# Kernel tuning notes

Measured on AMD Instinct MI355X. Metric: run time of the kernel, lower is better.

## Reference

```python
import jax, jax.numpy as jnp
import numpy as np
import math

NHEADS = 8


def pos_encoding_2d(d_model, H, W):
    dm = d_model // 2
    div = jnp.exp(jnp.arange(0, dm, 2, dtype=jnp.float32) * (-math.log(10000.0) / dm))  # [dm//2]
    pw = jnp.arange(W, dtype=jnp.float32)[:, None] * div  # [W, dm//2]
    ph = jnp.arange(H, dtype=jnp.float32)[:, None] * div  # [H, dm//2]
    pe = jnp.zeros((d_model, H, W), jnp.float32)
    pe = pe.at[0:dm:2].set(jnp.broadcast_to(jnp.sin(pw).T[:, None, :], (dm // 2, H, W)))
    pe = pe.at[1:dm:2].set(jnp.broadcast_to(jnp.cos(pw).T[:, None, :], (dm // 2, H, W)))
    pe = pe.at[dm::2].set(jnp.broadcast_to(jnp.sin(ph).T[:, :, None], (dm // 2, H, W)))
    pe = pe.at[dm + 1::2].set(jnp.broadcast_to(jnp.cos(ph).T[:, :, None], (dm // 2, H, W)))
    return pe


def conv_same(x, w, b):
    y = jax.lax.conv_general_dilated(x, w, (1, 1), 'SAME',
                                     dimension_numbers=('NCHW', 'OIHW', 'NCHW'))
    return y + b[None, :, None, None]


def layernorm(x, g, b, eps=1e-5):
    mu = x.mean(-1, keepdims=True)
    var = ((x - mu) ** 2).mean(-1, keepdims=True)
    return (x - mu) / jnp.sqrt(var + eps) * g + b


def setup_inputs() -> dict:
    key = jax.random.key(0)
    B, C, H, W = 8, 256, 32, 32
    KQV, NH, K = 64, NHEADS, 3
    ks = jax.random.split(key, 16)
    s_conv = 1.0 / math.sqrt(C * K * K)
    s_lin = 1.0 / math.sqrt(NH * KQV)
    s_ff = 1.0 / math.sqrt(C)
    return {
        'x': jax.random.normal(ks[0], (B, C, H, W), jnp.float32),
        'Wk': jax.random.normal(ks[1], (NH * KQV, C, K, K), jnp.float32) * s_conv,
        'bk': jax.random.normal(ks[2], (NH * KQV,), jnp.float32) * s_conv,
        'Wq': jax.random.normal(ks[3], (NH * KQV, C, K, K), jnp.float32) * s_conv,
        'bq': jax.random.normal(ks[4], (NH * KQV,), jnp.float32) * s_conv,
        'Wv': jax.random.normal(ks[5], (NH * KQV, C, K, K), jnp.float32) * s_conv,
        'bv': jax.random.normal(ks[6], (NH * KQV,), jnp.float32) * s_conv,
        'Wproj': jax.random.normal(ks[7], (C, NH * KQV), jnp.float32) * s_lin,
        'bproj': jax.random.normal(ks[8], (C,), jnp.float32) * s_lin,
        'ln_g': jnp.ones((C,), jnp.float32),
        'ln_b': jnp.zeros((C,), jnp.float32),
        'W1': jax.random.normal(ks[9], (C, C), jnp.float32) * s_ff,
        'b1': jax.random.normal(ks[10], (C,), jnp.float32) * s_ff,
        'W2': jax.random.normal(ks[11], (C, C), jnp.float32) * s_ff,
        'b2': jax.random.normal(ks[12], (C,), jnp.float32) * s_ff,
    }


def reference(x, Wk, bk, Wq, bq, Wv, bv, Wproj, bproj, ln_g, ln_b, W1, b1, W2, b2):
    B, C, H, W = x.shape
    N = H * W
    pe = pos_encoding_2d(C, H, W)
    xp = x + pe[None]                                   # [B,C,H,W]
    xflat = xp.reshape(B, C, N).transpose(0, 2, 1)      # [B,N,C]

    def heads(w, b):
        return conv_same(xp, w, b).reshape(B, NHEADS, -1, N)  # [B,h,c,N]

    k = heads(Wk, bk)
    q = heads(Wq, bq)
    v = heads(Wv, bv)
    scores = jnp.einsum('bhcn,bhcm->bhnm', k, q) / N    # K^T Q / N, [B,h,N,N]
    sm = jax.nn.softmax(scores, axis=1)                 # Softmax2d -> over HEAD dim (faithful)
    att = jnp.einsum('bhnm,bhcm->bhnc', sm, v)          # [B,h,N,c]
    att = att.transpose(0, 2, 3, 1).reshape(B, N, -1)   # [B,N,c*h] (channel-major, head-minor)
    attproj = att @ Wproj.T + bproj                     # [B,N,C]
    addnormed = layernorm(xflat + attproj, ln_g, ln_b)
    h1 = addnormed @ W1.T + b1
    h1 = jnp.where(h1 > 0, h1, 0.1 * h1)                # LeakyReLU(0.1)
    h2 = h1 @ W2.T + b2
    out = layernorm(h2 + addnormed, ln_g, ln_b)         # same LN params reused (faithful)
    return out.transpose(0, 2, 1).reshape(B, C, H, W)
```

## Files before the change

### kernel.cpp

```cpp
#include <hip/hip_runtime.h>
#include <stdint.h>

typedef __attribute__((ext_vector_type(8))) short short8;
typedef __attribute__((ext_vector_type(4))) short s16x4;
typedef __attribute__((ext_vector_type(4))) float f32x4;

#define DEVI __device__ __forceinline__

#if __has_builtin(__builtin_amdgcn_mfma_f32_16x16x16_bf16)
#define MFMA16(a, b, c) __builtin_amdgcn_mfma_f32_16x16x16_bf16(a, b, c, 0, 0, 0)
#else
#define MFMA16(a, b, c) __builtin_amdgcn_mfma_f32_16x16x16bf16_1k(a, b, c, 0, 0, 0)
#endif

DEVI unsigned short f2bf(float f) {
  union { float f; uint32_t u; } v; v.f = f;
  return (unsigned short)((v.u + 0x7fffu + ((v.u >> 16) & 1u)) >> 16);
}

DEVI float bf2f(uint32_t hi16) {
  union { uint32_t u; float f; } v; v.u = hi16;
  return v.f;
}

DEVI uint32_t pkbf(float a, float b) {
  union { float f; uint32_t u; } x, y; x.f = a; y.f = b;
  return ((x.u + 0x8000u) >> 16) | (((y.u + 0x8000u) >> 16) << 16);
}

DEVI void gload_lds16(const void* g, void* l) {
  __builtin_amdgcn_global_load_lds(
      (const __attribute__((address_space(1))) uint32_t*)g,
      (__attribute__((address_space(3))) uint32_t*)l, 16, 0, 0);
}

__global__ void k_petab(float* __restrict__ T, float* __restrict__ zp) {
  int c = threadIdx.x;
  zp[c] = 0.0f;
  int idx = ((c >= 128) ? c - 128 : c) >> 1;
  float freq = expf(-(float)idx * (logf(10000.0f) / 64.0f));
  for (int p = 0; p < 32; ++p) {
    float ang = (float)p * freq;
    T[c * 32 + p] = (c & 1) ? cosf(ang) : sinf(ang);
  }
}

__global__ __launch_bounds__(256) void k_xpt(const float* __restrict__ x,
                                             const float* __restrict__ T,
                                             unsigned short* __restrict__ xpt_bf,
                                             float* __restrict__ xpt_f) {
  __shared__ __align__(16) float tile[32][36];
  const int b = blockIdx.z, c0 = blockIdx.x * 32, n0 = blockIdx.y * 32;
  const int t = threadIdx.x;
  {
    const int cl = t >> 3, ng = (t & 7) * 4;
    const int c = c0 + cl;
    float4 v = *(const float4*)(x + ((size_t)b * 256 + c) * 1024 + n0 + ng);
    float p0, p1, p2, p3;
    if (c < 128) {
      p0 = T[c * 32 + ng + 0]; p1 = T[c * 32 + ng + 1];
      p2 = T[c * 32 + ng + 2]; p3 = T[c * 32 + ng + 3];
    } else {
      p0 = p1 = p2 = p3 = T[c * 32 + (n0 >> 5)];
    }
    tile[ng + 0][cl] = v.x + p0;
    tile[ng + 1][cl] = v.y + p1;
    tile[ng + 2][cl] = v.z + p2;
    tile[ng + 3][cl] = v.w + p3;
  }
  __syncthreads();
  {
    const int nl = t >> 3, cg = (t & 7) * 4;
    float o0 = tile[nl][cg + 0], o1 = tile[nl][cg + 1];
    float o2 = tile[nl][cg + 2], o3 = tile[nl][cg + 3];
    size_t row = (size_t)b * 1024 + n0 + nl;
    *(float4*)(xpt_f + row * 256 + c0 + cg) = make_float4(o0, o1, o2, o3);
    uint32_t lo = (uint32_t)f2bf(o0) | ((uint32_t)f2bf(o1) << 16);
    uint32_t hi = (uint32_t)f2bf(o2) | ((uint32_t)f2bf(o3) << 16);
    *(uint2*)(xpt_bf + row * 256 + c0 + cg) = make_uint2(lo, hi);
  }
}

__global__ void k_packw(const float* __restrict__ Wk, const float* __restrict__ Wq,
                        const float* __restrict__ Wv, unsigned short* __restrict__ Wpack) {
  int i = blockIdx.x * 256 + threadIdx.x;
  if (i >= 1536 * 2304) return;
  int o = i / 2304, kn = i % 2304;
  int ci = kn & 255, khw = kn >> 8;
  const float* src = (o < 512) ? Wk : ((o < 1024) ? Wq : Wv);
  int oo = o & 511;
  Wpack[i] = f2bf(src[((size_t)oo * 256 + ci) * 9 + khw]);
}

__global__ void k_packmisc(const float* __restrict__ bk, const float* __restrict__ bq,
                           const float* __restrict__ bv, const float* __restrict__ Wproj,
                           const float* __restrict__ W1, const float* __restrict__ W2,
                           float* __restrict__ bias_kqv, unsigned short* __restrict__ WprojP,
                           unsigned short* __restrict__ W1b, unsigned short* __restrict__ W2b) {
  int i = blockIdx.x * 256 + threadIdx.x;
  if (i < 1536)
    bias_kqv[i] = (i < 512) ? bk[i] : ((i < 1024) ? bq[i - 512] : bv[i - 1024]);
  if (i < 131072) {
    int j = i >> 9, f = i & 511;
    int h = f >> 6, c = f & 63;
    WprojP[i] = f2bf(Wproj[(size_t)j * 512 + c * 8 + h]);
  }
  if (i < 65536) {
    W1b[i] = f2bf(W1[i]);
    W2b[i] = f2bf(W2[i]);
  }
}

__global__ __launch_bounds__(256, 2) void k_gemm_conv(const unsigned short* __restrict__ xpt,
                                                      const unsigned short* __restrict__ Wp,
                                                      unsigned short* __restrict__ kqv,
                                                      const float* __restrict__ bias,
                                                      const char* __restrict__ zp) {
  __shared__ __align__(16) unsigned short As[2][128 * 64];
  __shared__ __align__(16) unsigned short Bs[2][128 * 64];
  const int tid = threadIdx.x, l = tid & 63, w = tid >> 6;
  const int wm = w >> 1, wn = w & 1, g = l >> 4, ln = l & 15;
  const int m0 = blockIdx.x * 128, n0 = blockIdx.y * 128;
  const int swz = (l & 7) ^ (l >> 3);

  int rA[4];
  const char* pAbase[4];
  const char* pA[4];
#pragma unroll
  for (int j = 0; j < 4; ++j) {
    int r = m0 + (w * 4 + j) * 8 + (l >> 3);
    rA[j] = r;
    pAbase[j] = (const char*)xpt + ((size_t)r * 256 + swz * 8) * 2;
  }
  const char* pB[4];
#pragma unroll
  for (int j = 0; j < 4; ++j) {
    int r = n0 + (w * 4 + j) * 8 + (l >> 3);
    pB[j] = (const char*)Wp + ((size_t)r * 2304 + swz * 8) * 2;
  }

  f32x4 acc[4][4] = {};

  auto setA = [&](int khw) {
    int d3 = (khw * 11) >> 5;
    int dy = d3 - 1, dx = khw - d3 * 3 - 1;
    int off = (dy * 32 + dx) * 512;
#pragma unroll
    for (int j = 0; j < 4; ++j) {
      int y = ((rA[j] >> 5) & 31) + dy;
      int x = (rA[j] & 31) + dx;
      pA[j] = (((unsigned)y < 32u) && ((unsigned)x < 32u)) ? (pAbase[j] + off) : zp;
    }
  };
  auto STAGE = [&](int buf) {
#pragma unroll
    for (int j = 0; j < 4; ++j) {
      gload_lds16(pA[j], (char*)As + buf * 16384 + (w * 4 + j) * 1024);
      pA[j] += 128;
    }
#pragma unroll
    for (int j = 0; j < 4; ++j) {
      gload_lds16(pB[j], (char*)Bs + buf * 16384 + (w * 4 + j) * 1024);
      pB[j] += 128;
    }
  };
  auto COMPUTE = [&](int buf) {
    const char* Ab2 = (const char*)As + buf * 16384;
    const char* Bb2 = (const char*)Bs + buf * 16384;
#pragma unroll
    for (int kk = 0; kk < 2; ++kk) {
      short8 af[4], bfr[4];
#pragma unroll
      for (int fm = 0; fm < 4; ++fm)
        af[fm] = *(const short8*)(Ab2 + (wm * 64 + fm * 16 + ln) * 128 +
                                  (((kk * 4 + g) ^ (ln & 7)) * 16));
#pragma unroll
      for (int fn = 0; fn < 4; ++fn)
        bfr[fn] = *(const short8*)(Bb2 + (wn * 64 + fn * 16 + ln) * 128 +
                                   (((kk * 4 + g) ^ (ln & 7)) * 16));
#pragma unroll
      for (int fm = 0; fm < 4; ++fm)
#pragma unroll
        for (int fn = 0; fn < 4; ++fn)
          acc[fm][fn] = __builtin_amdgcn_mfma_f32_16x16x32_bf16(af[fm], bfr[fn], acc[fm][fn], 0, 0, 0);
    }
  };

  setA(0);
  STAGE(0);
#pragma unroll
  for (int s = 0; s < 36; ++s) {
    const int buf = s & 1;
    if (s < 35) {
      if (((s + 1) & 3) == 0) setA((s + 1) >> 2);
      STAGE(buf ^ 1);
      asm volatile("s_waitcnt vmcnt(8)" ::: "memory");
    } else {
      asm volatile("s_waitcnt vmcnt(0)" ::: "memory");
    }
    __builtin_amdgcn_s_barrier();
    __builtin_amdgcn_sched_barrier(0);
    COMPUTE(buf);
    asm volatile("s_waitcnt lgkmcnt(0)" ::: "memory");
    __builtin_amdgcn_s_barrier();
    __builtin_amdgcn_sched_barrier(0);
  }

#pragma unroll
  for (int fm = 0; fm < 4; ++fm)
#pragma unroll
    for (int fn = 0; fn < 4; ++fn) {
      int col = n0 + wn * 64 + fn * 16 + ln;
      float bb = bias[col];
#pragma unroll
      for (int r = 0; r < 4; ++r) {
        int row = m0 + wm * 64 + fm * 16 + g * 4 + r;
        kqv[(size_t)row * 1536 + col] = f2bf(acc[fm][fn][r] + bb);
      }
    }
}

template <int EPI>
__global__ __launch_bounds__(256) void k_gemm64(const unsigned short* __restrict__ A,
                                                const unsigned short* __restrict__ B,
                                                void* __restrict__ Cout,
                                                const float* __restrict__ bias,
                                                const float* __restrict__ resid,
                                                int N, int K) {
  __shared__ __align__(16) unsigned short As[128 * 64];
  __shared__ __align__(16) unsigned short Bs[64 * 64];
  const int tid = threadIdx.x, l = tid & 63, w = tid >> 6;
  const int g = l >> 4, ln = l & 15;
  const int m0 = blockIdx.x * 128, n0 = blockIdx.y * 64;
  const int swz = (l & 7) ^ (l >> 3);
  f32x4 acc[2][4] = {};

  for (int kt = 0; kt < K; kt += 64) {
#pragma unroll
    for (int j = 0; j < 4; ++j) {
      int seg = w * 4 + j;
      int r8 = seg * 8 + (l >> 3);
      gload_lds16((const char*)A + ((size_t)(m0 + r8) * K + kt + swz * 8) * 2,
                  (char*)As + seg * 1024);
    }
#pragma unroll
    for (int j = 0; j < 2; ++j) {
      int seg = w * 2 + j;
      int r8 = seg * 8 + (l >> 3);
      gload_lds16((const char*)B + ((size_t)(n0 + r8) * K + kt + swz * 8) * 2,
                  (char*)Bs + seg * 1024);
    }
    __syncthreads();
#pragma unroll
    for (int kk = 0; kk < 2; ++kk) {
      short8 af[2], bfr[4];
#pragma unroll
      for (int fm = 0; fm < 2; ++fm)
        af[fm] = *(const short8*)((const char*)As + (w * 32 + fm * 16 + ln) * 128 +
                                  (((kk * 4 + g) ^ (ln & 7)) * 16));
#pragma unroll
      for (int fn = 0; fn < 4; ++fn)
        bfr[fn] = *(const short8*)((const char*)Bs + (fn * 16 + ln) * 128 +
                                   (((kk * 4 + g) ^ (ln & 7)) * 16));
#pragma unroll
      for (int fm = 0; fm < 2; ++fm)
#pragma unroll
        for (int fn = 0; fn < 4; ++fn)
          acc[fm][fn] = __builtin_amdgcn_mfma_f32_16x16x32_bf16(af[fm], bfr[fn], acc[fm][fn], 0, 0, 0);
    }
    __syncthreads();
  }

#pragma unroll
  for (int fm = 0; fm < 2; ++fm)
#pragma unroll
    for (int fn = 0; fn < 4; ++fn)
#pragma unroll
      for (int r = 0; r < 4; ++r) {
        int row = m0 + w * 32 + fm * 16 + g * 4 + r;
        int col = n0 + fn * 16 + ln;
        float v = acc[fm][fn][r] + bias[col];
        size_t cidx = (size_t)row * N + col;
        if (EPI == 2) {
          ((float*)Cout)[cidx] = v + resid[cidx];
        } else {
          v = (v > 0.f) ? v : 0.1f * v;
          ((unsigned short*)Cout)[cidx] = f2bf(v);
        }
      }
}

__global__ __launch_bounds__(512, 4) void k_attn(const unsigned short* __restrict__ kqv,
                                                 unsigned short* __restrict__ part) {
  __shared__ __align__(16) unsigned short Qs[16][512];
  __shared__ __align__(16) unsigned short Vlin[16][512];
  __shared__ __align__(16) unsigned short Vs[32][16][16];
  __shared__ __align__(16) float sums[4][2][64][4];
  const int tid = threadIdx.x, l = tid & 63, w = tid >> 6;
  const int g = l >> 4, ln = l & 15;
  const int nt = w & 1, hg = w >> 1;
  const int id = blockIdx.x;
  const int b = id & 7, ng = (id >> 3) & 31, ch = id >> 8;
  const int n0 = ng * 32 + nt * 16;
  const int m_base = ch * 512;
  const size_t rowBase = (size_t)b * 1024;
  const float SC = 1.0f / 1024.0f;

  short8 ak[2][2];
#pragma unroll
  for (int hl = 0; hl < 2; ++hl)
#pragma unroll
    for (int kk = 0; kk < 2; ++kk)
      ak[hl][kk] = *(const short8*)&kqv[(rowBase + n0 + ln) * 1536 +
                                        (hg * 2 + hl) * 64 + kk * 32 + g * 8];

  f32x4 acc[2][4] = {};

  auto STAGE = [&](int m0s) {
#pragma unroll
    for (int i = 0; i < 2; ++i) {
      int row = w * 2 + i;
      const unsigned short* src = kqv + (rowBase + m0s + row) * 1536;
      gload_lds16(src + 512 + ((l ^ (row & 7)) * 8), (char*)Qs + row * 1024);
      gload_lds16(src + 1024 + ((l ^ (row & 7)) * 8), (char*)Vlin + row * 1024);
    }
  };

  STAGE(m_base);
  asm volatile("s_waitcnt vmcnt(0)" ::: "memory");
  __builtin_amdgcn_s_barrier();
  __builtin_amdgcn_sched_barrier(0);

  const uint32_t vsBase = (uint32_t)(uintptr_t)&Vs[0][0][0] + l * 8;

  for (int s = 0; s < 32; ++s) {
    {
      const int tm = l & 15;
#pragma unroll
      for (int i = 0; i < 2; ++i) {
        int tch = (l >> 4) + w * 4 + i * 32;
        short8 tv = *(const short8*)((const char*)Vlin + tm * 1024 +
                                     ((tch ^ (tm & 7)) * 16));
        *(short8*)((char*)Vs + (tch >> 1) * 512 + tm * 32 + (tch & 1) * 16) = tv;
      }
    }

    f32x4 sv[2] = {};
#pragma unroll
    for (int kk = 0; kk < 2; ++kk)
#pragma unroll
      for (int hl = 0; hl < 2; ++hl) {
        int chq = (hg * 2 + hl) * 8 + kk * 4 + g;
        short8 qa = *(const short8*)((const char*)Qs + ln * 1024 +
                                     ((chq ^ (ln & 7)) * 16));
        sv[hl] = __builtin_amdgcn_mfma_f32_16x16x32_bf16(qa, ak[hl][kk], sv[hl], 0, 0, 0);
      }

    f32x4 e0, e1, ps;
#pragma unroll
    for (int j = 0; j < 4; ++j) {
      e0[j] = __expf(sv[0][j] * SC);
      e1[j] = __expf(sv[1][j] * SC);
      ps[j] = e0[j] + e1[j];
    }
    *(f32x4*)&sums[hg][nt][l][0] = ps;
    asm volatile("s_waitcnt lgkmcnt(0)" ::: "memory");
    __builtin_amdgcn_s_barrier();
    __builtin_amdgcn_sched_barrier(0);

    if (s < 31) STAGE(m_base + (s + 1) * 16);

    f32x4 tot = ps;
#pragma unroll
    for (int d = 1; d < 4; ++d) {
      f32x4 o = *(const f32x4*)&sums[(hg + d) & 3][nt][l][0];
      tot[0] += o[0]; tot[1] += o[1]; tot[2] += o[2]; tot[3] += o[3];
    }
    f32x4 inv;
#pragma unroll
    for (int j = 0; j < 4; ++j) inv[j] = 1.0f / tot[j];

    s16x4 vf[8];
#pragma unroll
    for (int hl = 0; hl < 2; ++hl) {
      uint32_t ah = vsBase + (hg * 2 + hl) * 2048;
      asm volatile("ds_read_b64_tr_b16 %0, %1" : "=v"(vf[hl * 4 + 0]) : "v"(ah));
      asm volatile("ds_read_b64_tr_b16 %0, %1 offset:512" : "=v"(vf[hl * 4 + 1]) : "v"(ah));
      asm volatile("ds_read_b64_tr_b16 %0, %1 offset:1024" : "=v"(vf[hl * 4 + 2]) : "v"(ah));
      asm volatile("ds_read_b64_tr_b16 %0, %1 offset:1536" : "=v"(vf[hl * 4 + 3]) : "v"(ah));
    }
    asm volatile("s_waitcnt lgkmcnt(0)" ::: "memory");
    __builtin_amdgcn_sched_barrier(0);
    union { uint32_t u[2]; s16x4 v4; } pc0, pc1;
    pc0.u[0] = pkbf(e0[0] * inv[0], e0[1] * inv[1]);
    pc0.u[1] = pkbf(e0[2] * inv[2], e0[3] * inv[3]);
    pc1.u[0] = pkbf(e1[0] * inv[0], e1[1] * inv[1]);
    pc1.u[1] = pkbf(e1[2] * inv[2], e1[3] * inv[3]);
#pragma unroll
    for (int cf = 0; cf < 4; ++cf) {
      acc[0][cf] = MFMA16(vf[cf], pc0.v4, acc[0][cf]);
      acc[1][cf] = MFMA16(vf[4 + cf], pc1.v4, acc[1][cf]);
    }

    asm volatile("s_waitcnt vmcnt(0)" ::: "memory");
    __builtin_amdgcn_s_barrier();
    __builtin_amdgcn_sched_barrier(0);
  }

  const size_t outBase = (size_t)ch * 8192 * 512 + (rowBase + n0 + ln) * 512;
#pragma unroll
  for (int hl = 0; hl < 2; ++hl)
#pragma unroll
    for (int cf = 0; cf < 4; ++cf)
#pragma unroll
      for (int r2 = 0; r2 < 2; ++r2) {
        int c = (hg * 2 + hl) * 64 + cf * 16 + g * 4 + r2 * 2;
        uint32_t u = (uint32_t)f2bf(acc[hl][cf][2 * r2]) |
                     ((uint32_t)f2bf(acc[hl][cf][2 * r2 + 1]) << 16);
        *(uint32_t*)&part[outBase + c] = u;
      }
}

__global__ __launch_bounds__(256) void k_reduce2(const unsigned short* __restrict__ part,
                                                 unsigned short* __restrict__ att) {
  size_t i8 = ((size_t)blockIdx.x * 256 + threadIdx.x) * 8;
  float o[8] = {0.f, 0.f, 0.f, 0.f, 0.f, 0.f, 0.f, 0.f};
#pragma unroll
  for (int p = 0; p < 2; ++p) {
    uint4 u = *(const uint4*)&part[(size_t)p * 8192 * 512 + i8];
    uint32_t a[4] = {u.x, u.y, u.z, u.w};
#pragma unroll
    for (int j = 0; j < 4; ++j) {
      o[2 * j] += bf2f(a[j] << 16);
      o[2 * j + 1] += bf2f(a[j] & 0xffff0000u);
    }
  }
  uint32_t r0 = (uint32_t)f2bf(o[0]) | ((uint32_t)f2bf(o[1]) << 16);
  uint32_t r1 = (uint32_t)f2bf(o[2]) | ((uint32_t)f2bf(o[3]) << 16);
  uint32_t r2 = (uint32_t)f2bf(o[4]) | ((uint32_t)f2bf(o[5]) << 16);
  uint32_t r3 = (uint32_t)f2bf(o[6]) | ((uint32_t)f2bf(o[7]) << 16);
  *(uint4*)&att[i8] = make_uint4(r0, r1, r2, r3);
}

template <int MODE>
__global__ __launch_bounds__(256) void k_ln(const float* __restrict__ in,
                                            const float* __restrict__ g,
                                            const float* __restrict__ bta,
                                            float* __restrict__ out_f,
                                            unsigned short* __restrict__ out_b) {
  const int l = threadIdx.x & 63, w = threadIdx.x >> 6;
  const size_t row = (size_t)blockIdx.x * 4 + w;
  float4 xv = *(const float4*)(in + row * 256 + l * 4);
  float s = xv.x + xv.y + xv.z + xv.w;
  float q = xv.x * xv.x + xv.y * xv.y + xv.z * xv.z + xv.w * xv.w;
#pragma unroll
  for (int o = 1; o < 64; o <<= 1) {
    s += __shfl_xor(s, o, 64);
    q += __shfl_xor(q, o, 64);
  }
  float mu = s * (1.0f / 256.0f);
  float var = q * (1.0f / 256.0f) - mu * mu;
  float rstd = rsqrtf(var + 1e-5f);
  float4 gv = *(const float4*)(g + l * 4);
  float4 bv = *(const float4*)(bta + l * 4);
  float o0 = (xv.x - mu) * rstd * gv.x + bv.x;
  float o1 = (xv.y - mu) * rstd * gv.y + bv.y;
  float o2 = (xv.z - mu) * rstd * gv.z + bv.z;
  float o3 = (xv.w - mu) * rstd * gv.w + bv.w;
  *(float4*)(out_f + row * 256 + l * 4) = make_float4(o0, o1, o2, o3);
  if (MODE == 0) {
    uint32_t lo = (uint32_t)f2bf(o0) | ((uint32_t)f2bf(o1) << 16);
    uint32_t hi = (uint32_t)f2bf(o2) | ((uint32_t)f2bf(o3) << 16);
    *(uint2*)(out_b + row * 256 + l * 4) = make_uint2(lo, hi);
  }
}

__global__ __launch_bounds__(256) void k_transout(const float* __restrict__ in,
                                                  float* __restrict__ out) {
  __shared__ __align__(16) float tile[32][36];
  const int b = blockIdx.z, c0 = blockIdx.x * 32, n0 = blockIdx.y * 32;
  const int t = threadIdx.x;
  {
    const int nl = t >> 3, cg = (t & 7) * 4;
    float4 v = *(const float4*)(in + ((size_t)b * 1024 + n0 + nl) * 256 + c0 + cg);
    tile[cg + 0][nl] = v.x;
    tile[cg + 1][nl] = v.y;
    tile[cg + 2][nl] = v.z;
    tile[cg + 3][nl] = v.w;
  }
  __syncthreads();
  {
    const int cl = t >> 3, ng = (t & 7) * 4;
    float4 o = make_float4(tile[cl][ng + 0], tile[cl][ng + 1], tile[cl][ng + 2], tile[cl][ng + 3]);
    *(float4*)(out + ((size_t)b * 256 + c0 + cl) * 1024 + n0 + ng) = o;
  }
}

extern "C" void kernel_launch(void* const* d_in, const int* in_sizes, int n_in,
                              void* d_out, int out_size, void* d_ws, size_t ws_size,
                              hipStream_t stream) {
  const float* x     = (const float*)d_in[0];
  const float* Wk    = (const float*)d_in[1];
  const float* bk    = (const float*)d_in[2];
  const float* Wq    = (const float*)d_in[3];
  const float* bq    = (const float*)d_in[4];
  const float* Wv    = (const float*)d_in[5];
  const float* bv    = (const float*)d_in[6];
  const float* Wproj = (const float*)d_in[7];
  const float* bproj = (const float*)d_in[8];
  const float* ln_g  = (const float*)d_in[9];
  const float* ln_b  = (const float*)d_in[10];
  const float* W1    = (const float*)d_in[11];
  const float* b1    = (const float*)d_in[12];
  const float* W2    = (const float*)d_in[13];
  const float* b2    = (const float*)d_in[14];

  char* ws = (char*)d_ws;
  constexpr size_t OFF_XPTB  = 0;
  constexpr size_t OFF_XPTF  = OFF_XPTB  + (size_t)8192 * 256 * 2;
  constexpr size_t OFF_WPACK = OFF_XPTF  + (size_t)8192 * 256 * 4;
  constexpr size_t OFF_BIAS  = OFF_WPACK + (size_t)1536 * 2304 * 2;
  constexpr size_t OFF_WPROJ = OFF_BIAS  + (size_t)1536 * 4;
  constexpr size_t OFF_W1B   = OFF_WPROJ + (size_t)256 * 512 * 2;
  constexpr size_t OFF_W2B   = OFF_W1B   + (size_t)256 * 256 * 2;
  constexpr size_t OFF_PET   = OFF_W2B   + (size_t)256 * 256 * 2;
  constexpr size_t OFF_ZERO  = OFF_PET   + (size_t)256 * 32 * 4;
  constexpr size_t OFF_KQV   = OFF_ZERO  + 1024;
  constexpr size_t OFF_ATT   = OFF_KQV   + (size_t)8192 * 1536 * 2;
  constexpr size_t OFF_X     = OFF_ATT   + (size_t)8192 * 512 * 2;
  constexpr size_t OFF_PART  = OFF_X;
  constexpr size_t OFF_Y1    = OFF_X;
  constexpr size_t OFF_ADDNF = OFF_Y1    + (size_t)8192 * 256 * 4;
  constexpr size_t OFF_ADDNB = OFF_ADDNF + (size_t)8192 * 256 * 4;
  constexpr size_t OFF_H1    = OFF_ADDNB + (size_t)8192 * 256 * 2;
  constexpr size_t OFF_H2    = OFF_H1    + (size_t)8192 * 256 * 2;

  (void)in_sizes; (void)n_in; (void)out_size; (void)ws_size;

  const char* zp = (const char*)(ws + OFF_ZERO);

  k_petab<<<1, 256, 0, stream>>>((float*)(ws + OFF_PET), (float*)(ws + OFF_ZERO));
  k_xpt<<<dim3(8, 32, 8), 256, 0, stream>>>(x, (const float*)(ws + OFF_PET),
                                            (unsigned short*)(ws + OFF_XPTB),
                                            (float*)(ws + OFF_XPTF));
  k_packw<<<(1536 * 2304 + 255) / 256, 256, 0, stream>>>(Wk, Wq, Wv,
                                                         (unsigned short*)(ws + OFF_WPACK));
  k_packmisc<<<512, 256, 0, stream>>>(bk, bq, bv, Wproj, W1, W2,
                                      (float*)(ws + OFF_BIAS),
                                      (unsigned short*)(ws + OFF_WPROJ),
                                      (unsigned short*)(ws + OFF_W1B),
                                      (unsigned short*)(ws + OFF_W2B));
  k_gemm_conv<<<dim3(64, 12), 256, 0, stream>>>(
      (const unsigned short*)(ws + OFF_XPTB), (const unsigned short*)(ws + OFF_WPACK),
      (unsigned short*)(ws + OFF_KQV), (const float*)(ws + OFF_BIAS), zp);
  k_attn<<<dim3(512), 512, 0, stream>>>((const unsigned short*)(ws + OFF_KQV),
                                        (unsigned short*)(ws + OFF_PART));
  k_reduce2<<<dim3(2048), 256, 0, stream>>>((const unsigned short*)(ws + OFF_PART),
                                            (unsigned short*)(ws + OFF_ATT));
  k_gemm64<2><<<dim3(64, 4), 256, 0, stream>>>(
      (const unsigned short*)(ws + OFF_ATT), (const unsigned short*)(ws + OFF_WPROJ),
      ws + OFF_Y1, bproj, (const float*)(ws + OFF_XPTF), 256, 512);
  k_ln<0><<<2048, 256, 0, stream>>>((const float*)(ws + OFF_Y1), ln_g, ln_b,
                                    (float*)(ws + OFF_ADDNF), (unsigned short*)(ws + OFF_ADDNB));
  k_gemm64<3><<<dim3(64, 4), 256, 0, stream>>>(
      (const unsigned short*)(ws + OFF_ADDNB), (const unsigned short*)(ws + OFF_W1B),
      ws + OFF_H1, b1, nullptr, 256, 256);
  k_gemm64<2><<<dim3(64, 4), 256, 0, stream>>>(
      (const unsigned short*)(ws + OFF_H1), (const unsigned short*)(ws + OFF_W2B),
      ws + OFF_H2, b2, (const float*)(ws + OFF_ADDNF), 256, 256);
  k_ln<1><<<2048, 256, 0, stream>>>((const float*)(ws + OFF_H2), ln_g, ln_b,
                                    (float*)(ws + OFF_Y1), nullptr);
  k_transout<<<dim3(8, 32, 8), 256, 0, stream>>>((const float*)(ws + OFF_Y1), (float*)d_out);
}
```

Measured before the change: 213.1 us.

## Fuse split-K reduce into projection GEMM and fuse FFN2, LayerNorm and transpose

```diff
diff --git a/kernel.cpp b/kernel.cpp
--- a/kernel.cpp
+++ b/kernel.cpp
@@ -81,33 +81,37 @@
   }
 }
 
-__global__ void k_packw(const float* __restrict__ Wk, const float* __restrict__ Wq,
-                        const float* __restrict__ Wv, unsigned short* __restrict__ Wpack) {
-  int i = blockIdx.x * 256 + threadIdx.x;
-  if (i >= 1536 * 2304) return;
-  int o = i / 2304, kn = i % 2304;
-  int ci = kn & 255, khw = kn >> 8;
-  const float* src = (o < 512) ? Wk : ((o < 1024) ? Wq : Wv);
-  int oo = o & 511;
-  Wpack[i] = f2bf(src[((size_t)oo * 256 + ci) * 9 + khw]);
-}
-
-__global__ void k_packmisc(const float* __restrict__ bk, const float* __restrict__ bq,
-                           const float* __restrict__ bv, const float* __restrict__ Wproj,
-                           const float* __restrict__ W1, const float* __restrict__ W2,
-                           float* __restrict__ bias_kqv, unsigned short* __restrict__ WprojP,
-                           unsigned short* __restrict__ W1b, unsigned short* __restrict__ W2b) {
-  int i = blockIdx.x * 256 + threadIdx.x;
-  if (i < 1536)
-    bias_kqv[i] = (i < 512) ? bk[i] : ((i < 1024) ? bq[i - 512] : bv[i - 1024]);
-  if (i < 131072) {
-    int j = i >> 9, f = i & 511;
-    int h = f >> 6, c = f & 63;
-    WprojP[i] = f2bf(Wproj[(size_t)j * 512 + c * 8 + h]);
-  }
-  if (i < 65536) {
-    W1b[i] = f2bf(W1[i]);
-    W2b[i] = f2bf(W2[i]);
+__global__ void k_packall(const float* __restrict__ Wk, const float* __restrict__ Wq,
+                          const float* __restrict__ Wv, const float* __restrict__ bk,
+                          const float* __restrict__ bq, const float* __restrict__ bv,
+                          const float* __restrict__ Wproj, const float* __restrict__ W1,
+                          const float* __restrict__ W2, unsigned short* __restrict__ Wpack,
+                          float* __restrict__ bias_kqv, unsigned short* __restrict__ WprojP,
+                          unsigned short* __restrict__ W1b, unsigned short* __restrict__ W2b) {
+  int bid = blockIdx.x;
+  if (bid < 13824) {
+    int i = bid * 256 + threadIdx.x;
+    if (i >= 1536 * 2304) return;
+    int o = i / 2304, kn = i % 2304;
+    int ci = kn & 255, khw = kn >> 8;
+    const float* src = (o < 512) ? Wk : ((o < 1024) ? Wq : Wv);
+    int oo = o & 511;
+    Wpack[i] = f2bf(src[((size_t)oo * 256 + ci) * 9 + khw]);
+  } else {
+    int i = (bid - 13824) * 256 + threadIdx.x;
+    if (i < 1536)
+      bias_kqv[i] = (i < 512) ? bk[i] : ((i < 1024) ? bq[i - 512] : bv[i - 1024]);
+    {
+      int j = i >> 9, f = i & 511;
+      int h = f >> 6, c = f & 63;
+      unsigned short v = f2bf(Wproj[(size_t)j * 512 + c * 8 + h]);
+      WprojP[(size_t)j * 1024 + f] = v;
+      WprojP[(size_t)j * 1024 + 512 + f] = v;
+    }
+    if (i < 65536) {
+      W1b[i] = f2bf(W1[i]);
+      W2b[i] = f2bf(W2[i]);
+    }
   }
 }
 
@@ -220,7 +224,7 @@
     }
 }
 
-template <int EPI>
+template <int EPI, bool ASPLIT>
 __global__ __launch_bounds__(256) void k_gemm64(const unsigned short* __restrict__ A,
                                                 const unsigned short* __restrict__ B,
                                                 void* __restrict__ Cout,
@@ -240,8 +244,13 @@
     for (int j = 0; j < 4; ++j) {
       int seg = w * 4 + j;
       int r8 = seg * 8 + (l >> 3);
-      gload_lds16((const char*)A + ((size_t)(m0 + r8) * K + kt + swz * 8) * 2,
-                  (char*)As + seg * 1024);
+      const char* src;
+      if (ASPLIT)
+        src = (const char*)A + (((size_t)(kt >> 9) * 8192 * 512) +
+                                (size_t)(m0 + r8) * 512 + (kt & 511) + swz * 8) * 2;
+      else
+        src = (const char*)A + ((size_t)(m0 + r8) * K + kt + swz * 8) * 2;
+      gload_lds16(src, (char*)As + seg * 1024);
     }
 #pragma unroll
     for (int j = 0; j < 2; ++j) {
@@ -421,33 +430,11 @@
       }
 }
 
-__global__ __launch_bounds__(256) void k_reduce2(const unsigned short* __restrict__ part,
-                                                 unsigned short* __restrict__ att) {
-  size_t i8 = ((size_t)blockIdx.x * 256 + threadIdx.x) * 8;
-  float o[8] = {0.f, 0.f, 0.f, 0.f, 0.f, 0.f, 0.f, 0.f};
-#pragma unroll
-  for (int p = 0; p < 2; ++p) {
-    uint4 u = *(const uint4*)&part[(size_t)p * 8192 * 512 + i8];
-    uint32_t a[4] = {u.x, u.y, u.z, u.w};
-#pragma unroll
-    for (int j = 0; j < 4; ++j) {
-      o[2 * j] += bf2f(a[j] << 16);
-      o[2 * j + 1] += bf2f(a[j] & 0xffff0000u);
-    }
-  }
-  uint32_t r0 = (uint32_t)f2bf(o[0]) | ((uint32_t)f2bf(o[1]) << 16);
-  uint32_t r1 = (uint32_t)f2bf(o[2]) | ((uint32_t)f2bf(o[3]) << 16);
-  uint32_t r2 = (uint32_t)f2bf(o[4]) | ((uint32_t)f2bf(o[5]) << 16);
-  uint32_t r3 = (uint32_t)f2bf(o[6]) | ((uint32_t)f2bf(o[7]) << 16);
-  *(uint4*)&att[i8] = make_uint4(r0, r1, r2, r3);
-}
-
-template <int MODE>
-__global__ __launch_bounds__(256) void k_ln(const float* __restrict__ in,
-                                            const float* __restrict__ g,
-                                            const float* __restrict__ bta,
-                                            float* __restrict__ out_f,
-                                            unsigned short* __restrict__ out_b) {
+__global__ __launch_bounds__(256) void k_ln0(const float* __restrict__ in,
+                                             const float* __restrict__ g,
+                                             const float* __restrict__ bta,
+                                             float* __restrict__ out_f,
+                                             unsigned short* __restrict__ out_b) {
   const int l = threadIdx.x & 63, w = threadIdx.x >> 6;
   const size_t row = (size_t)blockIdx.x * 4 + w;
   float4 xv = *(const float4*)(in + row * 256 + l * 4);
@@ -468,31 +455,109 @@
   float o2 = (xv.z - mu) * rstd * gv.z + bv.z;
   float o3 = (xv.w - mu) * rstd * gv.w + bv.w;
   *(float4*)(out_f + row * 256 + l * 4) = make_float4(o0, o1, o2, o3);
-  if (MODE == 0) {
-    uint32_t lo = (uint32_t)f2bf(o0) | ((uint32_t)f2bf(o1) << 16);
-    uint32_t hi = (uint32_t)f2bf(o2) | ((uint32_t)f2bf(o3) << 16);
-    *(uint2*)(out_b + row * 256 + l * 4) = make_uint2(lo, hi);
-  }
-}
-
-__global__ __launch_bounds__(256) void k_transout(const float* __restrict__ in,
-                                                  float* __restrict__ out) {
-  __shared__ __align__(16) float tile[32][36];
-  const int b = blockIdx.z, c0 = blockIdx.x * 32, n0 = blockIdx.y * 32;
-  const int t = threadIdx.x;
-  {
-    const int nl = t >> 3, cg = (t & 7) * 4;
-    float4 v = *(const float4*)(in + ((size_t)b * 1024 + n0 + nl) * 256 + c0 + cg);
-    tile[cg + 0][nl] = v.x;
-    tile[cg + 1][nl] = v.y;
-    tile[cg + 2][nl] = v.z;
-    tile[cg + 3][nl] = v.w;
-  }
+  uint32_t lo = (uint32_t)f2bf(o0) | ((uint32_t)f2bf(o1) << 16);
+  uint32_t hi = (uint32_t)f2bf(o2) | ((uint32_t)f2bf(o3) << 16);
+  *(uint2*)(out_b + row * 256 + l * 4) = make_uint2(lo, hi);
+}
+
+__global__ __launch_bounds__(256) void k_ffn2out(const unsigned short* __restrict__ h1,
+                                                 const unsigned short* __restrict__ W2b,
+                                                 const float* __restrict__ b2,
+                                                 const float* __restrict__ addnf,
+                                                 const float* __restrict__ lg,
+                                                 const float* __restrict__ lb,
+                                                 float* __restrict__ out) {
+  __shared__ __align__(16) unsigned short As[32 * 64];
+  __shared__ __align__(16) unsigned short Bs[256 * 64];
+  __shared__ __align__(16) float Tt[256][33];
+  __shared__ float rsum[4][32][2];
+  const int tid = threadIdx.x, l = tid & 63, w = tid >> 6;
+  const int g4 = l >> 4, ln = l & 15;
+  const int m0 = blockIdx.x * 32;
+  const int swz = (l & 7) ^ (l >> 3);
+  f32x4 acc[2][4] = {};
+
+  for (int kt = 0; kt < 256; kt += 64) {
+    gload_lds16((const char*)h1 + ((size_t)(m0 + w * 8 + (l >> 3)) * 256 + kt + swz * 8) * 2,
+                (char*)As + w * 1024);
+#pragma unroll
+    for (int j = 0; j < 8; ++j) {
+      int seg = w * 8 + j;
+      gload_lds16((const char*)W2b + ((size_t)(seg * 8 + (l >> 3)) * 256 + kt + swz * 8) * 2,
+                  (char*)Bs + seg * 1024);
+    }
+    __syncthreads();
+#pragma unroll
+    for (int kk = 0; kk < 2; ++kk) {
+      short8 af[2], bfr[4];
+#pragma unroll
+      for (int fm = 0; fm < 2; ++fm)
+        af[fm] = *(const short8*)((const char*)As + (fm * 16 + ln) * 128 +
+                                  (((kk * 4 + g4) ^ (ln & 7)) * 16));
+#pragma unroll
+      for (int fn = 0; fn < 4; ++fn)
+        bfr[fn] = *(const short8*)((const char*)Bs + (w * 64 + fn * 16 + ln) * 128 +
+                                   (((kk * 4 + g4) ^ (ln & 7)) * 16));
+#pragma unroll
+      for (int fm = 0; fm < 2; ++fm)
+#pragma unroll
+        for (int fn = 0; fn < 4; ++fn)
+          acc[fm][fn] = __builtin_amdgcn_mfma_f32_16x16x32_bf16(af[fm], bfr[fn], acc[fm][fn], 0, 0, 0);
+    }
+    __syncthreads();
+  }
+
+  float vals[2][4][4];
+#pragma unroll
+  for (int fm = 0; fm < 2; ++fm)
+#pragma unroll
+    for (int r = 0; r < 4; ++r) {
+      int row_l = fm * 16 + g4 * 4 + r;
+      float s = 0.f, q = 0.f;
+#pragma unroll
+      for (int fn = 0; fn < 4; ++fn) {
+        int col = w * 64 + fn * 16 + ln;
+        float v = acc[fm][fn][r] + b2[col] + addnf[(size_t)(m0 + row_l) * 256 + col];
+        vals[fm][fn][r] = v;
+        s += v;
+        q += v * v;
+      }
+#pragma unroll
+      for (int o = 1; o < 16; o <<= 1) {
+        s += __shfl_xor(s, o, 64);
+        q += __shfl_xor(q, o, 64);
+      }
+      if (ln == 0) {
+        rsum[w][row_l][0] = s;
+        rsum[w][row_l][1] = q;
+      }
+    }
   __syncthreads();
-  {
-    const int cl = t >> 3, ng = (t & 7) * 4;
-    float4 o = make_float4(tile[cl][ng + 0], tile[cl][ng + 1], tile[cl][ng + 2], tile[cl][ng + 3]);
-    *(float4*)(out + ((size_t)b * 256 + c0 + cl) * 1024 + n0 + ng) = o;
+
+#pragma unroll
+  for (int fm = 0; fm < 2; ++fm)
+#pragma unroll
+    for (int r = 0; r < 4; ++r) {
+      int row_l = fm * 16 + g4 * 4 + r;
+      float s = rsum[0][row_l][0] + rsum[1][row_l][0] + rsum[2][row_l][0] + rsum[3][row_l][0];
+      float q = rsum[0][row_l][1] + rsum[1][row_l][1] + rsum[2][row_l][1] + rsum[3][row_l][1];
+      float mu = s * (1.0f / 256.0f);
+      float rstd = rsqrtf(q * (1.0f / 256.0f) - mu * mu + 1e-5f);
+#pragma unroll
+      for (int fn = 0; fn < 4; ++fn) {
+        int col = w * 64 + fn * 16 + ln;
+        Tt[col][row_l] = (vals[fm][fn][r] - mu) * rstd * lg[col] + lb[col];
+      }
+    }
+  __syncthreads();
+
+  const int bimg = m0 >> 10, nn0 = m0 & 1023;
+#pragma unroll
+  for (int i = 0; i < 8; ++i) {
+    int c = i * 32 + (tid >> 3);
+    int ng = (tid & 7) * 4;
+    float4 o = make_float4(Tt[c][ng], Tt[c][ng + 1], Tt[c][ng + 2], Tt[c][ng + 3]);
+    *(float4*)&out[((size_t)bimg * 256 + c) * 1024 + nn0 + ng] = o;
   }
 }
 
@@ -521,19 +586,16 @@
   constexpr size_t OFF_WPACK = OFF_XPTF  + (size_t)8192 * 256 * 4;
   constexpr size_t OFF_BIAS  = OFF_WPACK + (size_t)1536 * 2304 * 2;
   constexpr size_t OFF_WPROJ = OFF_BIAS  + (size_t)1536 * 4;
-  constexpr size_t OFF_W1B   = OFF_WPROJ + (size_t)256 * 512 * 2;
+  constexpr size_t OFF_W1B   = OFF_WPROJ + (size_t)256 * 1024 * 2;
   constexpr size_t OFF_W2B   = OFF_W1B   + (size_t)256 * 256 * 2;
   constexpr size_t OFF_PET   = OFF_W2B   + (size_t)256 * 256 * 2;
   constexpr size_t OFF_ZERO  = OFF_PET   + (size_t)256 * 32 * 4;
   constexpr size_t OFF_KQV   = OFF_ZERO  + 1024;
-  constexpr size_t OFF_ATT   = OFF_KQV   + (size_t)8192 * 1536 * 2;
-  constexpr size_t OFF_X     = OFF_ATT   + (size_t)8192 * 512 * 2;
-  constexpr size_t OFF_PART  = OFF_X;
-  constexpr size_t OFF_Y1    = OFF_X;
+  constexpr size_t OFF_PART  = OFF_KQV   + (size_t)8192 * 1536 * 2;
+  constexpr size_t OFF_Y1    = OFF_PART  + (size_t)2 * 8192 * 512 * 2;
   constexpr size_t OFF_ADDNF = OFF_Y1    + (size_t)8192 * 256 * 4;
   constexpr size_t OFF_ADDNB = OFF_ADDNF + (size_t)8192 * 256 * 4;
   constexpr size_t OFF_H1    = OFF_ADDNB + (size_t)8192 * 256 * 2;
-  constexpr size_t OFF_H2    = OFF_H1    + (size_t)8192 * 256 * 2;
 
   (void)in_sizes; (void)n_in; (void)out_size; (void)ws_size;
 
@@ -543,32 +605,27 @@
   k_xpt<<<dim3(8, 32, 8), 256, 0, stream>>>(x, (const float*)(ws + OFF_PET),
                                             (unsigned short*)(ws + OFF_XPTB),
                                             (float*)(ws + OFF_XPTF));
-  k_packw<<<(1536 * 2304 + 255) / 256, 256, 0, stream>>>(Wk, Wq, Wv,
-                                                         (unsigned short*)(ws + OFF_WPACK));
-  k_packmisc<<<512, 256, 0, stream>>>(bk, bq, bv, Wproj, W1, W2,
-                                      (float*)(ws + OFF_BIAS),
-                                      (unsigned short*)(ws + OFF_WPROJ),
-                                      (unsigned short*)(ws + OFF_W1B),
-                                      (unsigned short*)(ws + OFF_W2B));
+  k_packall<<<14336, 256, 0, stream>>>(Wk, Wq, Wv, bk, bq, bv, Wproj, W1, W2,
+                                       (unsigned short*)(ws + OFF_WPACK),
+                                       (float*)(ws + OFF_BIAS),
+                                       (unsigned short*)(ws + OFF_WPROJ),
+                                       (unsigned short*)(ws + OFF_W1B),
+                                       (unsigned short*)(ws + OFF_W2B));
   k_gemm_conv<<<dim3(64, 12), 256, 0, stream>>>(
       (const unsigned short*)(ws + OFF_XPTB), (const unsigned short*)(ws + OFF_WPACK),
       (unsigned short*)(ws + OFF_KQV), (const float*)(ws + OFF_BIAS), zp);
   k_attn<<<dim3(512), 512, 0, stream>>>((const unsigned short*)(ws + OFF_KQV),
                                         (unsigned short*)(ws + OFF_PART));
-  k_reduce2<<<dim3(2048), 256, 0, stream>>>((const unsigned short*)(ws + OFF_PART),
-                                            (unsigned short*)(ws + OFF_ATT));
-  k_gemm64<2><<<dim3(64, 4), 256, 0, stream>>>(
-      (const unsigned short*)(ws + OFF_ATT), (const unsigned short*)(ws + OFF_WPROJ),
-      ws + OFF_Y1, bproj, (const float*)(ws + OFF_XPTF), 256, 512);
-  k_ln<0><<<2048, 256, 0, stream>>>((const float*)(ws + OFF_Y1), ln_g, ln_b,
-                                    (float*)(ws + OFF_ADDNF), (unsigned short*)(ws + OFF_ADDNB));
-  k_gemm64<3><<<dim3(64, 4), 256, 0, stream>>>(
+  k_gemm64<2, true><<<dim3(64, 4), 256, 0, stream>>>(
+      (const unsigned short*)(ws + OFF_PART), (const unsigned short*)(ws + OFF_WPROJ),
+      ws + OFF_Y1, bproj, (const float*)(ws + OFF_XPTF), 256, 1024);
+  k_ln0<<<2048, 256, 0, stream>>>((const float*)(ws + OFF_Y1), ln_g, ln_b,
+                                  (float*)(ws + OFF_ADDNF), (unsigned short*)(ws + OFF_ADDNB));
+  k_gemm64<3, false><<<dim3(64, 4), 256, 0, stream>>>(
       (const unsigned short*)(ws + OFF_ADDNB), (const unsigned short*)(ws + OFF_W1B),
       ws + OFF_H1, b1, nullptr, 256, 256);
-  k_gemm64<2><<<dim3(64, 4), 256, 0, stream>>>(
-      (const unsigned short*)(ws + OFF_H1), (const unsigned short*)(ws + OFF_W2B),
-      ws + OFF_H2, b2, (const float*)(ws + OFF_ADDNF), 256, 256);
-  k_ln<1><<<2048, 256, 0, stream>>>((const float*)(ws + OFF_H2), ln_g, ln_b,
-                                    (float*)(ws + OFF_Y1), nullptr);
-  k_transout<<<dim3(8, 32, 8), 256, 0, stream>>>((const float*)(ws + OFF_Y1), (float*)d_out);
-}
+  k_ffn2out<<<256, 256, 0, stream>>>((const unsigned short*)(ws + OFF_H1),
+                                     (const unsigned short*)(ws + OFF_W2B), b2,
+                                     (const float*)(ws + OFF_ADDNF), ln_g, ln_b,
+                                     (float*)d_out);
+}
```

Result: faster. 206.2 us (-3.2%).
